# Performance work log

Hardware: AMD Instinct MI355X
Metric: run time of the kernel (lower is better)

Reference implementation:

```python
import jax, jax.numpy as jnp
import numpy as np

V = 100000
E = 1600000
NODE_IN = 128
EDGE_IN = 50
H = 50  # all hidden/out sizes default to 50


def _linear_params(key, fan_in, fan_out):
    kw, kb = jax.random.split(key)
    bound = 1.0 / np.sqrt(fan_in)
    w = jax.random.uniform(kw, (fan_in, fan_out), jnp.float32, -bound, bound)
    b = jax.random.uniform(kb, (fan_out,), jnp.float32, -bound, bound)
    return w, b


def setup_inputs() -> dict:
    key = jax.random.key(0)
    ks = jax.random.split(key, 11)
    node_feats = jax.random.normal(ks[0], (V, NODE_IN), jnp.float32)
    edge_feats = jax.random.normal(ks[1], (E, EDGE_IN), jnp.float32)
    src = jax.random.randint(ks[2], (E,), 0, V, jnp.int32)
    dst = jax.random.randint(ks[3], (E,), 0, V, jnp.int32)
    w_n2n, b_n2n = _linear_params(ks[4], NODE_IN, H)
    w_e2n, b_e2n = _linear_params(ks[5], EDGE_IN, H)
    w_upd_n, b_upd_n = _linear_params(ks[6], 2 * H, H)
    w_l, b_l = _linear_params(ks[7], NODE_IN, H)
    w_r, b_r = _linear_params(ks[8], NODE_IN, H)
    w_e2e, b_e2e = _linear_params(ks[9], EDGE_IN, H)
    w_upd_e, b_upd_e = _linear_params(ks[10], 3 * H, H)
    return {
        "node_feats": node_feats, "edge_feats": edge_feats,
        "src": src, "dst": dst,
        "w_n2n": w_n2n, "b_n2n": b_n2n,
        "w_e2n": w_e2n, "b_e2n": b_e2n,
        "w_upd_n": w_upd_n, "b_upd_n": b_upd_n,
        "w_l": w_l, "b_l": b_l,
        "w_r": w_r, "b_r": b_r,
        "w_e2e": w_e2e, "b_e2e": b_e2e,
        "w_upd_e": w_upd_e, "b_upd_e": b_upd_e,
    }


def reference(node_feats, edge_feats, src, dst,
              w_n2n, b_n2n, w_e2n, b_e2n, w_upd_n, b_upd_n,
              w_l, b_l, w_r, b_r, w_e2e, b_e2e, w_upd_e, b_upd_e):
    relu = jax.nn.relu
    num_nodes = node_feats.shape[0]
    # node update
    node_node = relu(node_feats @ w_n2n + b_n2n)                # (V, H)
    e2n = relu(edge_feats @ w_e2n + b_e2n)                      # (E, H)
    # copy_edge + sum: scatter-sum edge messages onto destination nodes
    edge_node = jax.ops.segment_sum(e2n, dst, num_segments=num_nodes)  # (V, H)
    new_node = relu(jnp.concatenate([node_node, edge_node], axis=1) @ w_upd_n + b_upd_n)
    # edge update
    left = node_feats @ w_l + b_l                               # (V, H)
    right = node_feats @ w_r + b_r                              # (V, H)
    first = relu(left[src] + right[dst])                        # u_add_v(left, right)
    second = relu(right[src] + left[dst])                       # u_add_v(right, left)
    third = relu(edge_feats @ w_e2e + b_e2e)                    # (E, H)
    new_edge = relu(jnp.concatenate([first, second, third], axis=1) @ w_upd_e + b_upd_e)
    return new_node, new_edge
```

## Files before the change

kernel.cpp:

```cpp
#include <hip/hip_runtime.h>
#include <hip/hip_bf16.h>

typedef unsigned short u16;
typedef unsigned int   u32;

#define V_N 100000
#define E_N 1600000
#define NIN 128
#define EIN 50
#define HH  50
#define TPB 8

typedef __attribute__((ext_vector_type(8))) short bf16x8;
typedef __attribute__((ext_vector_type(4))) float f32x4;

__device__ __forceinline__ float bf2f(u16 u) {
    union { u32 i; float f; } v; v.i = ((u32)u) << 16; return v.f;
}
__device__ __forceinline__ u16 f2bf(float f) {
    union { float f; u32 i; } v; v.f = f;
    u32 x = v.i;
    return (u16)((x + 0x7fffu + ((x >> 16) & 1u)) >> 16);
}
__device__ __forceinline__ int swz(int row, int k) { return k ^ ((row & 7) << 3); }

__global__ __launch_bounds__(256, 3) void k_lr(
    const float* __restrict__ nf,
    const float* __restrict__ w1, const float* __restrict__ b1,
    const float* __restrict__ w2, const float* __restrict__ b2,
    u16* __restrict__ left, u16* __restrict__ right)
{
    __shared__ __align__(16) u16 sxa[64 * 128];
    __shared__ __align__(16) u16 swt[112 * 128];
    __shared__ float sb[112];

    const int tid  = threadIdx.x;
    const int row0 = blockIdx.x * 64;

    const float4* nf4 = (const float4*)nf;
    for (int i = tid; i < 64 * 32; i += 256) {
        const int row = i >> 5, k4 = (i & 31) << 2;
        float4 v = make_float4(0.f, 0.f, 0.f, 0.f);
        const int gr = row0 + row;
        if (gr < V_N) v = nf4[(size_t)gr * 32 + (k4 >> 2)];
        ushort4 p;
        p.x = f2bf(v.x); p.y = f2bf(v.y); p.z = f2bf(v.z); p.w = f2bf(v.w);
        *(ushort4*)&sxa[(row << 7) + swz(row, k4)] = p;
    }
    for (int i = tid; i < 112 * 128; i += 256) {
        const int n = i >> 7, k = i & 127;
        float v = 0.f;
        if (n < 50)       v = w1[k*50 + n];
        else if (n < 100) v = w2[k*50 + (n - 50)];
        swt[(n << 7) + swz(n, k)] = f2bf(v);
    }
    if (tid < 112)
        sb[tid] = (tid < 50) ? b1[tid] : (tid < 100 ? b2[tid - 50] : 0.f);
    __syncthreads();

    const int lane = tid & 63, wv = tid >> 6;
    const int frow = lane & 15;
    const int kofs = (lane >> 4) << 3;
    const int rbase = wv*16 + ((lane >> 4) << 2);
    const int arow  = wv*16 + frow;

    f32x4 zf = {0.f, 0.f, 0.f, 0.f};
    f32x4 acc[7];
    #pragma unroll
    for (int nt = 0; nt < 7; ++nt) acc[nt] = zf;

    #pragma unroll
    for (int kt = 0; kt < 4; ++kt) {
        bf16x8 a = *(const bf16x8*)&sxa[(arow << 7) + swz(arow, kt*32 + kofs)];
        #pragma unroll
        for (int nt = 0; nt < 7; ++nt) {
            const int nrow = nt*16 + frow;
            bf16x8 b = *(const bf16x8*)&swt[(nrow << 7) + swz(nrow, kt*32 + kofs)];
            acc[nt] = __builtin_amdgcn_mfma_f32_16x16x32_bf16(a, b, acc[nt], 0, 0, 0);
        }
    }
    #pragma unroll
    for (int nt = 0; nt < 7; ++nt) {
        const int g = nt*16 + frow;
        if (g < 100) {
            const float bias = sb[g];
            #pragma unroll
            for (int r = 0; r < 4; ++r) {
                const int gr = row0 + rbase + r;
                if (gr < V_N) {
                    const u16 o = f2bf(acc[nt][r] + bias);
                    if (g < 50) left [(size_t)gr*HH + g]      = o;
                    else        right[(size_t)gr*HH + g - 50] = o;
                }
            }
        }
    }
}

__global__ __launch_bounds__(256, 3) void k_edge(
    const float* __restrict__ ef,
    const int* __restrict__ src, const int* __restrict__ dst,
    const float* __restrict__ wA, const float* __restrict__ bA,
    const float* __restrict__ wB, const float* __restrict__ bB,
    const float* __restrict__ wU, const float* __restrict__ bU,
    const u16* __restrict__ left, const u16* __restrict__ right,
    float* __restrict__ edge_node_acc,
    float* __restrict__ out_edge)
{
    __shared__ __align__(16) u16 sint[64 * 192];
    __shared__ __align__(16) u16 wUt [64 * 192];
    __shared__ float sb[3 * HH];
    __shared__ int ssrc[64], sdst[64];

    const int tid  = threadIdx.x;
    const int lane = tid & 63, wv = tid >> 6;
    const int frow = lane & 15;
    const int kofs = (lane >> 4) << 3;
    const int rbase = wv*16 + ((lane >> 4) << 2);
    const int arow  = wv*16 + frow;

    {
        uint4 z = make_uint4(0,0,0,0);
        for (int i = tid; i < 64*192/8; i += 256) ((uint4*)sint)[i] = z;
    }
    for (int i = tid; i < 64*192; i += 256) {
        const int c = i / 192, kk = i - c*192;
        const int sec = kk >> 6, ko = kk & 63;
        u16 v = 0;
        if (c < 50 && ko < 50) v = f2bf(wU[(sec*50 + ko)*50 + c]);
        wUt[c*192 + swz(c, kk)] = v;
    }
    if (tid < 3*HH)
        sb[tid] = (tid < 50) ? bA[tid] : (tid < 100 ? bB[tid-50] : bU[tid-100]);

    bf16x8 bAf[2][4], bBf[2][4];
    #pragma unroll
    for (int kt = 0; kt < 2; ++kt) {
        #pragma unroll
        for (int nt = 0; nt < 4; ++nt) {
            union { bf16x8 v; u16 u[8]; } r1, r2;
            const int n = nt*16 + frow;
            #pragma unroll
            for (int j = 0; j < 8; ++j) {
                const int k = kt*32 + kofs + j;
                float v1 = 0.f, v2 = 0.f;
                if (k < 50 && n < 50) { v1 = wA[k*50 + n]; v2 = wB[k*50 + n]; }
                r1.u[j] = f2bf(v1); r2.u[j] = f2bf(v2);
            }
            bAf[kt][nt] = r1.v; bBf[kt][nt] = r2.v;
        }
    }
    __syncthreads();

    for (int tile = 0; tile < TPB; ++tile) {
        const int e0t = blockIdx.x * (64*TPB) + tile*64;

        if (tid < 64) { ssrc[tid] = src[e0t+tid]; sdst[tid] = dst[e0t+tid]; }
        __syncthreads();

        for (int t = tid; t < 64*25; t += 256) {
            const int e = t / 25, q = t - e*25, c = q*2;
            const int s = ssrc[e], d = sdst[e];
            const ushort2 ls  = *(const ushort2*)&left [(size_t)s*HH + c];
            const ushort2 rd_ = *(const ushort2*)&right[(size_t)d*HH + c];
            const ushort2 rs  = *(const ushort2*)&right[(size_t)s*HH + c];
            const ushort2 ld  = *(const ushort2*)&left [(size_t)d*HH + c];
            const u32 p1 = (u32)f2bf(fmaxf(bf2f(ls.x) + bf2f(rd_.x), 0.f))
                         | ((u32)f2bf(fmaxf(bf2f(ls.y) + bf2f(rd_.y), 0.f)) << 16);
            const u32 p2 = (u32)f2bf(fmaxf(bf2f(rs.x) + bf2f(ld.x), 0.f))
                         | ((u32)f2bf(fmaxf(bf2f(rs.y) + bf2f(ld.y), 0.f)) << 16);
            *(u32*)&sint[e*192 + swz(e, c)]      = p1;
            *(u32*)&sint[e*192 + swz(e, 64 + c)] = p2;
        }

        {
            f32x4 zf = {0.f, 0.f, 0.f, 0.f};
            f32x4 accA[4], accB[4];
            #pragma unroll
            for (int nt = 0; nt < 4; ++nt) { accA[nt] = zf; accB[nt] = zf; }
            const float* efr = ef + (size_t)(e0t + arow) * EIN;
            #pragma unroll
            for (int kt = 0; kt < 2; ++kt) {
                union { bf16x8 v; u16 u[8]; } a;
                #pragma unroll
                for (int p = 0; p < 4; ++p) {
                    const int k = kt*32 + kofs + 2*p;
                    float2 f = make_float2(0.f, 0.f);
                    if (k < 50) f = *(const float2*)&efr[k];
                    a.u[2*p]   = f2bf(f.x);
                    a.u[2*p+1] = f2bf(f.y);
                }
                #pragma unroll
                for (int nt = 0; nt < 4; ++nt) {
                    accA[nt] = __builtin_amdgcn_mfma_f32_16x16x32_bf16(a.v, bAf[kt][nt], accA[nt], 0, 0, 0);
                    accB[nt] = __builtin_amdgcn_mfma_f32_16x16x32_bf16(a.v, bBf[kt][nt], accB[nt], 0, 0, 0);
                }
            }
            #pragma unroll
            for (int nt = 0; nt < 4; ++nt) {
                const int c = nt*16 + frow;
                if (c < 50) {
                    const float ba = sb[c], bb = sb[HH + c];
                    #pragma unroll
                    for (int r = 0; r < 4; ++r) {
                        const int row = rbase + r;
                        const float v1 = fmaxf(accA[nt][r] + ba, 0.f);
                        atomicAdd(&edge_node_acc[(size_t)sdst[row]*HH + c], v1);
                        sint[row*192 + swz(row, 128 + c)] =
                            f2bf(fmaxf(accB[nt][r] + bb, 0.f));
                    }
                }
            }
        }
        __syncthreads();

        {
            f32x4 zf = {0.f, 0.f, 0.f, 0.f};
            f32x4 acc[4];
            #pragma unroll
            for (int nt = 0; nt < 4; ++nt) acc[nt] = zf;
            #pragma unroll
            for (int kt = 0; kt < 6; ++kt) {
                bf16x8 a = *(const bf16x8*)&sint[arow*192 + swz(arow, kt*32 + kofs)];
                #pragma unroll
                for (int nt = 0; nt < 4; ++nt) {
                    const int nrow = nt*16 + frow;
                    bf16x8 b = *(const bf16x8*)&wUt[nrow*192 + swz(nrow, kt*32 + kofs)];
                    acc[nt] = __builtin_amdgcn_mfma_f32_16x16x32_bf16(a, b, acc[nt], 0, 0, 0);
                }
            }
            #pragma unroll
            for (int nt = 0; nt < 4; ++nt) {
                const int c = nt*16 + frow;
                if (c < 50) {
                    const float bu = sb[2*HH + c];
                    #pragma unroll
                    for (int r = 0; r < 4; ++r) {
                        const int row = rbase + r;
                        out_edge[(size_t)(e0t + row)*HH + c] = fmaxf(acc[nt][r] + bu, 0.f);
                    }
                }
            }
        }
    }
}

__global__ __launch_bounds__(256, 2) void k_node_upd(
    const float* __restrict__ nf,
    const float* __restrict__ w_n2n, const float* __restrict__ b_n2n,
    const float* __restrict__ wU, const float* __restrict__ bU,
    float* __restrict__ node_out )
{
    __shared__ __align__(16) u16 smem[64*128 + 64*128];
    __shared__ __align__(16) u16 swu[64 * 192];
    __shared__ float sb[128];

    const int tid = threadIdx.x;
    const int n0  = blockIdx.x * 64;

    const float4* nf4 = (const float4*)nf;
    for (int i = tid; i < 64 * 32; i += 256) {
        const int row = i >> 5, k4 = (i & 31) << 2;
        float4 v = make_float4(0.f, 0.f, 0.f, 0.f);
        const int gr = n0 + row;
        if (gr < V_N) v = nf4[(size_t)gr * 32 + (k4 >> 2)];
        ushort4 p;
        p.x = f2bf(v.x); p.y = f2bf(v.y); p.z = f2bf(v.z); p.w = f2bf(v.w);
        *(ushort4*)&smem[(row << 7) + swz(row, k4)] = p;
    }
    for (int i = tid; i < 64 * 128; i += 256) {
        const int n = i >> 7, k = i & 127;
        const float v = (n < 50) ? w_n2n[k*50 + n] : 0.f;
        smem[8192 + (n << 7) + swz(n, k)] = f2bf(v);
    }
    for (int i = tid; i < 64 * 192; i += 256) {
        const int n = i / 192, kk = i - n*192;
        float v = 0.f;
        if (n < 50) {
            if (kk < 100)      v = wU[kk*50 + n];
            else if (kk < 150) v = wU[(kk - 50)*50 + n];
        }
        swu[n*192 + swz(n, kk)] = f2bf(v);
    }
    if (tid < 128) {
        float v = 0.f;
        if (tid < 50) v = b_n2n[tid];
        else if (tid >= 64 && tid < 114) v = bU[tid - 64];
        sb[tid] = v;
    }
    __syncthreads();

    const int lane = tid & 63, wv = tid >> 6;
    const int frow = lane & 15;
    const int kofs = (lane >> 4) << 3;
    const int rbase = wv*16 + ((lane >> 4) << 2);
    const int arow  = wv*16 + frow;

    f32x4 zf = {0.f, 0.f, 0.f, 0.f};

    f32x4 accB[4];
    #pragma unroll
    for (int nt = 0; nt < 4; ++nt) accB[nt] = zf;
    #pragma unroll
    for (int kt = 0; kt < 4; ++kt) {
        bf16x8 a = *(const bf16x8*)&smem[(arow << 7) + swz(arow, kt*32 + kofs)];
        #pragma unroll
        for (int nt = 0; nt < 4; ++nt) {
            const int nrow = nt*16 + frow;
            bf16x8 b = *(const bf16x8*)&smem[8192 + (nrow << 7) + swz(nrow, kt*32 + kofs)];
            accB[nt] = __builtin_amdgcn_mfma_f32_16x16x32_bf16(a, b, accB[nt], 0, 0, 0);
        }
    }
    __syncthreads();

    #pragma unroll
    for (int nt = 0; nt < 4; ++nt) {
        const int g = nt*16 + frow;
        if (g < 50) {
            const float bias = sb[g];
            #pragma unroll
            for (int r = 0; r < 4; ++r) {
                const int row = rbase + r;
                smem[row*192 + swz(row, g)] = f2bf(fmaxf(accB[nt][r] + bias, 0.f));
            }
        }
    }
    for (int i = tid; i < 4096; i += 256) {
        const int row = i >> 6, q = i & 63;
        if (q < 50) {
            float en = 0.f;
            const int gr = n0 + row;
            if (gr < V_N) en = node_out[(size_t)gr*HH + q];
            const u16 hi = f2bf(en);
            const u16 lo = f2bf(en - bf2f(hi));
            smem[row*192 + swz(row,  50 + q)] = hi;
            smem[row*192 + swz(row, 100 + q)] = lo;
        }
    }
    for (int i = tid; i < 4096; i += 256) {
        const int row = i >> 6, q = i & 63;
        if (q < 42) smem[row*192 + swz(row, 150 + q)] = 0;
    }
    __syncthreads();

    f32x4 accC[4];
    #pragma unroll
    for (int nt = 0; nt < 4; ++nt) accC[nt] = zf;
    #pragma unroll
    for (int kt = 0; kt < 6; ++kt) {
        bf16x8 a = *(const bf16x8*)&smem[arow*192 + swz(arow, kt*32 + kofs)];
        #pragma unroll
        for (int nt = 0; nt < 4; ++nt) {
            const int nrow = nt*16 + frow;
            bf16x8 b = *(const bf16x8*)&swu[nrow*192 + swz(nrow, kt*32 + kofs)];
            accC[nt] = __builtin_amdgcn_mfma_f32_16x16x32_bf16(a, b, accC[nt], 0, 0, 0);
        }
    }
    #pragma unroll
    for (int nt = 0; nt < 4; ++nt) {
        const int g = nt*16 + frow;
        if (g < 50) {
            const float bias = sb[64 + g];
            #pragma unroll
            for (int r = 0; r < 4; ++r) {
                const int gr = n0 + rbase + r;
                if (gr < V_N)
                    node_out[(size_t)gr*HH + g] = fmaxf(accC[nt][r] + bias, 0.f);
            }
        }
    }
}

extern "C" void kernel_launch(void* const* d_in, const int* in_sizes, int n_in,
                              void* d_out, int out_size, void* d_ws, size_t ws_size,
                              hipStream_t stream) {
    const float* nf    = (const float*)d_in[0];
    const float* ef    = (const float*)d_in[1];
    const int*   src   = (const int*)d_in[2];
    const int*   dst   = (const int*)d_in[3];
    const float* w_n2n = (const float*)d_in[4];  const float* b_n2n = (const float*)d_in[5];
    const float* w_e2n = (const float*)d_in[6];  const float* b_e2n = (const float*)d_in[7];
    const float* w_updn= (const float*)d_in[8];  const float* b_updn= (const float*)d_in[9];
    const float* w_l   = (const float*)d_in[10]; const float* b_l   = (const float*)d_in[11];
    const float* w_r   = (const float*)d_in[12]; const float* b_r   = (const float*)d_in[13];
    const float* w_e2e = (const float*)d_in[14]; const float* b_e2e = (const float*)d_in[15];
    const float* w_upde= (const float*)d_in[16]; const float* b_upde= (const float*)d_in[17];

    char* ws = (char*)d_ws;
    u16* left  = (u16*)ws;
    u16* right = (u16*)(ws + 10000000);

    float* out_node = (float*)d_out;
    float* out_edge = out_node + (size_t)V_N * HH;

    hipMemsetAsync(out_node, 0, (size_t)V_N * HH * sizeof(float), stream);

    k_lr<<<(V_N + 63)/64, 256, 0, stream>>>(nf, w_l, b_l, w_r, b_r, left, right);

    k_edge<<<E_N/(64*TPB), 256, 0, stream>>>(
        ef, src, dst, w_e2n, b_e2n, w_e2e, b_e2e, w_upde, b_upde,
        left, right, out_node, out_edge);

    k_node_upd<<<(V_N + 63)/64, 256, 0, stream>>>(
        nf, w_n2n, b_n2n, w_updn, b_updn, out_node);
}
```

Measured before the change: 1.275 ms.

## Batch gather loads into registers and coalesce weight staging loops

In the edge kernel, all node-embedding gathers for a tile and the edge-feature loads are issued up front into register arrays, then the sums and shared-memory stores follow. This is meant to expose more memory-level parallelism and hide gather latency. Separately, the weight-staging loops are re-indexed so consecutive threads read consecutive output columns, making the global weight reads coalesced. The cost is higher register pressure from the 7-element gather buffers, which may reduce occupancy.

Result: slower. 1.570 ms (+23.1%).

```diff
diff --git a/kernel.cpp b/kernel.cpp
--- a/kernel.cpp
+++ b/kernel.cpp
@@ -48,7 +48,7 @@
         *(ushort4*)&sxa[(row << 7) + swz(row, k4)] = p;
     }
     for (int i = tid; i < 112 * 128; i += 256) {
-        const int n = i >> 7, k = i & 127;
+        const int n = i % 112, k = i / 112;
         float v = 0.f;
         if (n < 50)       v = w1[k*50 + n];
         else if (n < 100) v = w2[k*50 + (n - 50)];
@@ -124,11 +124,11 @@
         for (int i = tid; i < 64*192/8; i += 256) ((uint4*)sint)[i] = z;
     }
     for (int i = tid; i < 64*192; i += 256) {
-        const int c = i / 192, kk = i - c*192;
+        const int n = i & 63, kk = i >> 6;
         const int sec = kk >> 6, ko = kk & 63;
         u16 v = 0;
-        if (c < 50 && ko < 50) v = f2bf(wU[(sec*50 + ko)*50 + c]);
-        wUt[c*192 + swz(c, kk)] = v;
+        if (n < 50 && ko < 50) v = f2bf(wU[(sec*50 + ko)*50 + n]);
+        wUt[n*192 + swz(n, kk)] = v;
     }
     if (tid < 3*HH)
         sb[tid] = (tid < 50) ? bA[tid] : (tid < 100 ? bB[tid-50] : bU[tid-100]);
@@ -158,19 +158,43 @@
         if (tid < 64) { ssrc[tid] = src[e0t+tid]; sdst[tid] = dst[e0t+tid]; }
         __syncthreads();
 
-        for (int t = tid; t < 64*25; t += 256) {
-            const int e = t / 25, q = t - e*25, c = q*2;
-            const int s = ssrc[e], d = sdst[e];
-            const ushort2 ls  = *(const ushort2*)&left [(size_t)s*HH + c];
-            const ushort2 rd_ = *(const ushort2*)&right[(size_t)d*HH + c];
-            const ushort2 rs  = *(const ushort2*)&right[(size_t)s*HH + c];
-            const ushort2 ld  = *(const ushort2*)&left [(size_t)d*HH + c];
-            const u32 p1 = (u32)f2bf(fmaxf(bf2f(ls.x) + bf2f(rd_.x), 0.f))
-                         | ((u32)f2bf(fmaxf(bf2f(ls.y) + bf2f(rd_.y), 0.f)) << 16);
-            const u32 p2 = (u32)f2bf(fmaxf(bf2f(rs.x) + bf2f(ld.x), 0.f))
-                         | ((u32)f2bf(fmaxf(bf2f(rs.y) + bf2f(ld.y), 0.f)) << 16);
-            *(u32*)&sint[e*192 + swz(e, c)]      = p1;
-            *(u32*)&sint[e*192 + swz(e, 64 + c)] = p2;
+        ushort2 gls[7], grd[7], grs[7], gld[7];
+        #pragma unroll
+        for (int it = 0; it < 7; ++it) {
+            const int t = tid + it*256;
+            if (t < 1600) {
+                const int e = t / 25, q = t - e*25, c = q*2;
+                const int s = ssrc[e], d = sdst[e];
+                gls[it] = *(const ushort2*)&left [(size_t)s*HH + c];
+                grd[it] = *(const ushort2*)&right[(size_t)d*HH + c];
+                grs[it] = *(const ushort2*)&right[(size_t)s*HH + c];
+                gld[it] = *(const ushort2*)&left [(size_t)d*HH + c];
+            }
+        }
+        const float* efr = ef + (size_t)(e0t + arow) * EIN;
+        float2 ge2[8];
+        #pragma unroll
+        for (int kt = 0; kt < 2; ++kt) {
+            #pragma unroll
+            for (int p = 0; p < 4; ++p) {
+                const int k = kt*32 + kofs + 2*p;
+                float2 f = make_float2(0.f, 0.f);
+                if (k < 50) f = *(const float2*)&efr[k];
+                ge2[kt*4 + p] = f;
+            }
+        }
+        #pragma unroll
+        for (int it = 0; it < 7; ++it) {
+            const int t = tid + it*256;
+            if (t < 1600) {
+                const int e = t / 25, q = t - e*25, c = q*2;
+                const u32 p1 = (u32)f2bf(fmaxf(bf2f(gls[it].x) + bf2f(grd[it].x), 0.f))
+                             | ((u32)f2bf(fmaxf(bf2f(gls[it].y) + bf2f(grd[it].y), 0.f)) << 16);
+                const u32 p2 = (u32)f2bf(fmaxf(bf2f(grs[it].x) + bf2f(gld[it].x), 0.f))
+                             | ((u32)f2bf(fmaxf(bf2f(grs[it].y) + bf2f(gld[it].y), 0.f)) << 16);
+                *(u32*)&sint[e*192 + swz(e, c)]      = p1;
+                *(u32*)&sint[e*192 + swz(e, 64 + c)] = p2;
+            }
         }
 
         {
@@ -178,15 +202,12 @@
             f32x4 accA[4], accB[4];
             #pragma unroll
             for (int nt = 0; nt < 4; ++nt) { accA[nt] = zf; accB[nt] = zf; }
-            const float* efr = ef + (size_t)(e0t + arow) * EIN;
             #pragma unroll
             for (int kt = 0; kt < 2; ++kt) {
                 union { bf16x8 v; u16 u[8]; } a;
                 #pragma unroll
                 for (int p = 0; p < 4; ++p) {
-                    const int k = kt*32 + kofs + 2*p;
-                    float2 f = make_float2(0.f, 0.f);
-                    if (k < 50) f = *(const float2*)&efr[k];
+                    const float2 f = ge2[kt*4 + p];
                     a.u[2*p]   = f2bf(f.x);
                     a.u[2*p+1] = f2bf(f.y);
                 }
@@ -269,12 +290,12 @@
         *(ushort4*)&smem[(row << 7) + swz(row, k4)] = p;
     }
     for (int i = tid; i < 64 * 128; i += 256) {
-        const int n = i >> 7, k = i & 127;
+        const int n = i & 63, k = i >> 6;
         const float v = (n < 50) ? w_n2n[k*50 + n] : 0.f;
         smem[8192 + (n << 7) + swz(n, k)] = f2bf(v);
     }
     for (int i = tid; i < 64 * 192; i += 256) {
-        const int n = i / 192, kk = i - n*192;
+        const int n = i & 63, kk = i >> 6;
         float v = 0.f;
         if (n < 50) {
             if (kk < 100)      v = wU[kk*50 + n];
```

## Fuse node_node projection into left/right GEMM and defer scatter atomics past barrier

Applied to the files above, without the earlier changes.

Adds k_lr3, which computes the left, right and node_node projections in a single 150-column MFMA GEMM over node features. The node_node result is stored as bf16 so the final node update (k_node3) no longer re-reads the fp32 node features or redoes that GEMM; it splits the aggregated edge sum into hi/lo bf16 parts to keep precision. In k_edge, the scatter atomicAdds are moved after the barrier, with destination indices held in registers, so they can overlap with the update GEMM. The fused path runs only when the workspace holds at least 30 MB, and it costs extra shared memory and lower occupancy in k_lr3.

Measured after the change: 1.287 ms. No clear change (+1.0%).

```diff
diff --git a/kernel.cpp b/kernel.cpp
--- a/kernel.cpp
+++ b/kernel.cpp
@@ -10,6 +10,7 @@
 #define EIN 50
 #define HH  50
 #define TPB 8
+#define NBLK 1563
 
 typedef __attribute__((ext_vector_type(8))) short bf16x8;
 typedef __attribute__((ext_vector_type(4))) float f32x4;
@@ -91,6 +92,87 @@
                     const u16 o = f2bf(acc[nt][r] + bias);
                     if (g < 50) left [(size_t)gr*HH + g]      = o;
                     else        right[(size_t)gr*HH + g - 50] = o;
+                }
+            }
+        }
+    }
+}
+
+__global__ __launch_bounds__(256, 2) void k_lr3(
+    const float* __restrict__ nf,
+    const float* __restrict__ w1, const float* __restrict__ b1,
+    const float* __restrict__ w2, const float* __restrict__ b2,
+    const float* __restrict__ wn, const float* __restrict__ bn,
+    u16* __restrict__ left, u16* __restrict__ right, u16* __restrict__ nn)
+{
+    __shared__ __align__(16) u16 sxa[64 * 128];
+    __shared__ __align__(16) u16 swt[160 * 128];
+    __shared__ float sb[160];
+
+    const int tid  = threadIdx.x;
+    const int row0 = blockIdx.x * 64;
+
+    const float4* nf4 = (const float4*)nf;
+    for (int i = tid; i < 64 * 32; i += 256) {
+        const int row = i >> 5, k4 = (i & 31) << 2;
+        float4 v = make_float4(0.f, 0.f, 0.f, 0.f);
+        const int gr = row0 + row;
+        if (gr < V_N) v = nf4[(size_t)gr * 32 + (k4 >> 2)];
+        ushort4 p;
+        p.x = f2bf(v.x); p.y = f2bf(v.y); p.z = f2bf(v.z); p.w = f2bf(v.w);
+        *(ushort4*)&sxa[(row << 7) + swz(row, k4)] = p;
+    }
+    for (int i = tid; i < 160 * 128; i += 256) {
+        const int n = i >> 7, k = i & 127;
+        float v = 0.f;
+        if (n < 50)       v = w1[k*50 + n];
+        else if (n < 100) v = w2[k*50 + (n - 50)];
+        else if (n < 150) v = wn[k*50 + (n - 100)];
+        swt[(n << 7) + swz(n, k)] = f2bf(v);
+    }
+    if (tid < 160) {
+        float v = 0.f;
+        if (tid < 50)       v = b1[tid];
+        else if (tid < 100) v = b2[tid - 50];
+        else if (tid < 150) v = bn[tid - 100];
+        sb[tid] = v;
+    }
+    __syncthreads();
+
+    const int lane = tid & 63, wv = tid >> 6;
+    const int frow = lane & 15;
+    const int kofs = (lane >> 4) << 3;
+    const int rbase = wv*16 + ((lane >> 4) << 2);
+    const int arow  = wv*16 + frow;
+
+    f32x4 zf = {0.f, 0.f, 0.f, 0.f};
+    f32x4 acc[10];
+    #pragma unroll
+    for (int nt = 0; nt < 10; ++nt) acc[nt] = zf;
+
+    #pragma unroll
+    for (int kt = 0; kt < 4; ++kt) {
+        bf16x8 a = *(const bf16x8*)&sxa[(arow << 7) + swz(arow, kt*32 + kofs)];
+        #pragma unroll
+        for (int nt = 0; nt < 10; ++nt) {
+            const int nrow = nt*16 + frow;
+            bf16x8 b = *(const bf16x8*)&swt[(nrow << 7) + swz(nrow, kt*32 + kofs)];
+            acc[nt] = __builtin_amdgcn_mfma_f32_16x16x32_bf16(a, b, acc[nt], 0, 0, 0);
+        }
+    }
+    #pragma unroll
+    for (int nt = 0; nt < 10; ++nt) {
+        const int g = nt*16 + frow;
+        if (g < 150) {
+            const float bias = sb[g];
+            #pragma unroll
+            for (int r = 0; r < 4; ++r) {
+                const int gr = row0 + rbase + r;
+                if (gr < V_N) {
+                    const float s = acc[nt][r] + bias;
+                    if (g < 50)       left [(size_t)gr*HH + g]       = f2bf(s);
+                    else if (g < 100) right[(size_t)gr*HH + g - 50]  = f2bf(s);
+                    else              nn   [(size_t)gr*HH + g - 100] = f2bf(fmaxf(s, 0.f));
                 }
             }
         }
@@ -173,9 +255,11 @@
             *(u32*)&sint[e*192 + swz(e, 64 + c)] = p2;
         }
 
+        f32x4 accA[4];
+        int rd_[4];
         {
             f32x4 zf = {0.f, 0.f, 0.f, 0.f};
-            f32x4 accA[4], accB[4];
+            f32x4 accB[4];
             #pragma unroll
             for (int nt = 0; nt < 4; ++nt) { accA[nt] = zf; accB[nt] = zf; }
             const float* efr = ef + (size_t)(e0t + arow) * EIN;
@@ -197,22 +281,34 @@
                 }
             }
             #pragma unroll
+            for (int r = 0; r < 4; ++r) rd_[r] = sdst[rbase + r];
+            #pragma unroll
             for (int nt = 0; nt < 4; ++nt) {
                 const int c = nt*16 + frow;
                 if (c < 50) {
-                    const float ba = sb[c], bb = sb[HH + c];
+                    const float bb = sb[HH + c];
                     #pragma unroll
                     for (int r = 0; r < 4; ++r) {
-                        const int row = rbase + r;
-                        const float v1 = fmaxf(accA[nt][r] + ba, 0.f);
-                        atomicAdd(&edge_node_acc[(size_t)sdst[row]*HH + c], v1);
-                        sint[row*192 + swz(row, 128 + c)] =
+                        sint[(rbase + r)*192 + swz(rbase + r, 128 + c)] =
                             f2bf(fmaxf(accB[nt][r] + bb, 0.f));
                     }
                 }
             }
         }
         __syncthreads();
+
+        #pragma unroll
+        for (int nt = 0; nt < 4; ++nt) {
+            const int c = nt*16 + frow;
+            if (c < 50) {
+                const float ba = sb[c];
+                #pragma unroll
+                for (int r = 0; r < 4; ++r) {
+                    atomicAdd(&edge_node_acc[(size_t)rd_[r]*HH + c],
+                              fmaxf(accA[nt][r] + ba, 0.f));
+                }
+            }
+        }
 
         {
             f32x4 zf = {0.f, 0.f, 0.f, 0.f};
@@ -249,7 +345,7 @@
     const float* __restrict__ nf,
     const float* __restrict__ w_n2n, const float* __restrict__ b_n2n,
     const float* __restrict__ wU, const float* __restrict__ bU,
-    float* __restrict__ node_out )
+    float* __restrict__ node_out)
 {
     __shared__ __align__(16) u16 smem[64*128 + 64*128];
     __shared__ __align__(16) u16 swu[64 * 192];
@@ -366,6 +462,89 @@
                 const int gr = n0 + rbase + r;
                 if (gr < V_N)
                     node_out[(size_t)gr*HH + g] = fmaxf(accC[nt][r] + bias, 0.f);
+            }
+        }
+    }
+}
+
+__global__ __launch_bounds__(256, 3) void k_node3(
+    const u16* __restrict__ nn,
+    const float* __restrict__ wU, const float* __restrict__ bU,
+    float* __restrict__ node_out)
+{
+    __shared__ __align__(16) u16 smem[64 * 192];
+    __shared__ __align__(16) u16 swu [64 * 192];
+    __shared__ float sb[64];
+
+    const int tid = threadIdx.x;
+    const int n0  = blockIdx.x * 64;
+
+    for (int i = tid; i < 64 * 192; i += 256) {
+        const int n = i / 192, kk = i - n*192;
+        float v = 0.f;
+        if (n < 50) {
+            if (kk < 100)      v = wU[kk*50 + n];
+            else if (kk < 150) v = wU[(kk - 50)*50 + n];
+        }
+        swu[n*192 + swz(n, kk)] = f2bf(v);
+    }
+    if (tid < 50) sb[tid] = bU[tid];
+    for (int i = tid; i < 4096; i += 256) {
+        const int row = i >> 6, q = i & 63;
+        if (q < 50) {
+            const int gr = n0 + row;
+            const u16 v = (gr < V_N) ? nn[(size_t)gr*HH + q] : (u16)0;
+            smem[row*192 + swz(row, q)] = v;
+        }
+    }
+    for (int i = tid; i < 4096; i += 256) {
+        const int row = i >> 6, q = i & 63;
+        if (q < 50) {
+            float en = 0.f;
+            const int gr = n0 + row;
+            if (gr < V_N) en = node_out[(size_t)gr*HH + q];
+            const u16 hi = f2bf(en);
+            const u16 lo = f2bf(en - bf2f(hi));
+            smem[row*192 + swz(row,  50 + q)] = hi;
+            smem[row*192 + swz(row, 100 + q)] = lo;
+        }
+    }
+    for (int i = tid; i < 4096; i += 256) {
+        const int row = i >> 6, q = i & 63;
+        if (q < 42) smem[row*192 + swz(row, 150 + q)] = 0;
+    }
+    __syncthreads();
+
+    const int lane = tid & 63, wv = tid >> 6;
+    const int frow = lane & 15;
+    const int kofs = (lane >> 4) << 3;
+    const int rbase = wv*16 + ((lane >> 4) << 2);
+    const int arow  = wv*16 + frow;
+
+    f32x4 zf = {0.f, 0.f, 0.f, 0.f};
+    f32x4 acc[4];
+    #pragma unroll
+    for (int nt = 0; nt < 4; ++nt) acc[nt] = zf;
+    #pragma unroll
+    for (int kt = 0; kt < 6; ++kt) {
+        bf16x8 a = *(const bf16x8*)&smem[arow*192 + swz(arow, kt*32 + kofs)];
+        #pragma unroll
+        for (int nt = 0; nt < 4; ++nt) {
+            const int nrow = nt*16 + frow;
+            bf16x8 b = *(const bf16x8*)&swu[nrow*192 + swz(nrow, kt*32 + kofs)];
+            acc[nt] = __builtin_amdgcn_mfma_f32_16x16x32_bf16(a, b, acc[nt], 0, 0, 0);
+        }
+    }
+    #pragma unroll
+    for (int nt = 0; nt < 4; ++nt) {
+        const int g = nt*16 + frow;
+        if (g < 50) {
+            const float bias = sb[g];
+            #pragma unroll
+            for (int r = 0; r < 4; ++r) {
+                const int gr = n0 + rbase + r;
+                if (gr < V_N)
+                    node_out[(size_t)gr*HH + g] = fmaxf(acc[nt][r] + bias, 0.f);
             }
         }
     }
@@ -389,18 +568,29 @@
     char* ws = (char*)d_ws;
     u16* left  = (u16*)ws;
     u16* right = (u16*)(ws + 10000000);
+    u16* nn    = (u16*)(ws + 20000000);
+    const bool fused = (ws_size >= 30000000);
 
     float* out_node = (float*)d_out;
     float* out_edge = out_node + (size_t)V_N * HH;
 
     hipMemsetAsync(out_node, 0, (size_t)V_N * HH * sizeof(float), stream);
 
-    k_lr<<<(V_N + 63)/64, 256, 0, stream>>>(nf, w_l, b_l, w_r, b_r, left, right);
+    if (fused) {
+        k_lr3<<<NBLK, 256, 0, stream>>>(nf, w_l, b_l, w_r, b_r, w_n2n, b_n2n,
+                                        left, right, nn);
+    } else {
+        k_lr<<<NBLK, 256, 0, stream>>>(nf, w_l, b_l, w_r, b_r, left, right);
+    }
 
     k_edge<<<E_N/(64*TPB), 256, 0, stream>>>(
         ef, src, dst, w_e2n, b_e2n, w_e2e, b_e2e, w_upde, b_upde,
         left, right, out_node, out_edge);
 
-    k_node_upd<<<(V_N + 63)/64, 256, 0, stream>>>(
-        nf, w_n2n, b_n2n, w_updn, b_updn, out_node);
-}
+    if (fused) {
+        k_node3<<<NBLK, 256, 0, stream>>>(nn, w_updn, b_updn, out_node);
+    } else {
+        k_node_upd<<<NBLK, 256, 0, stream>>>(nf, w_n2n, b_n2n, w_updn, b_updn,
+                                             out_node);
+    }
+}
```
